# Kernel tuning notes

Hardware: AMD Instinct MI355X
Metric: run time of the kernel (lower is better)

Reference implementation:

```python
import jax, jax.numpy as jnp
import numpy as np

B = 8
INPUT_DIM = 6670   # upper-triangle of 116x116 FC matrix (AAL atlas)
N = 116
FD = 16
HEADS = (8, 4, 1)
DIMS = (128, 256, 512)
NC = 2
THR = 0.5
EPS = 1e-5


def _glorot(key, shape):
    s = (2.0 / (shape[0] + shape[-1])) ** 0.5
    return jax.random.normal(key, shape, dtype=jnp.float32) * s


def setup_inputs() -> dict:
    key = jax.random.key(0)
    ks = iter(jax.random.split(key, 64))
    inp = {}
    inp['x'] = jax.random.normal(next(ks), (B, INPUT_DIM), dtype=jnp.float32)
    # DynamicGraphBuilder params
    inp['W_gb'] = _glorot(next(ks), (INPUT_DIM, N * N))
    inp['b_gb'] = jnp.zeros((N * N,), jnp.float32)
    inp['fe_W1'] = _glorot(next(ks), (2, 8)); inp['fe_b1'] = jnp.zeros((8,), jnp.float32)
    inp['fe_W2'] = _glorot(next(ks), (8, FD)); inp['fe_b2'] = jnp.zeros((FD,), jnp.float32)
    inp['ln_g'] = jnp.ones((FD,), jnp.float32); inp['ln_b'] = jnp.zeros((FD,), jnp.float32)
    # GATv2 layers
    prev = FD
    for l, (d, h) in enumerate(zip(DIMS, HEADS)):
        inp['Wl%d' % l] = _glorot(next(ks), (prev, h * d))
        inp['bl%d' % l] = jnp.zeros((h * d,), jnp.float32)
        inp['Wr%d' % l] = _glorot(next(ks), (prev, h * d))
        inp['br%d' % l] = jnp.zeros((h * d,), jnp.float32)
        inp['att%d' % l] = _glorot(next(ks), (h, d))
        inp['bias%d' % l] = jnp.zeros((h * d,), jnp.float32)
        prev = h * d
    # classifier
    inp['Wc1'] = _glorot(next(ks), (prev, 256)); inp['bc1'] = jnp.zeros((256,), jnp.float32)
    inp['bn_g'] = jnp.ones((256,), jnp.float32); inp['bn_b'] = jnp.zeros((256,), jnp.float32)
    inp['Wc2'] = _glorot(next(ks), (256, NC)); inp['bc2'] = jnp.zeros((NC,), jnp.float32)
    return inp


def _gatv2(hx, mask_st, Wl, bl, Wr, br, att, bias, heads, out_dim, self_loops):
    # mask_st[b, src, tgt] True if edge src->tgt exists (PyG flow source_to_target)
    Bn, Nn, _ = hx.shape
    if self_loops:  # PyG remove_self_loops + add_self_loops => diag forced present
        mask_st = mask_st | jnp.eye(Nn, dtype=bool)
    xl = (hx @ Wl + bl).reshape(Bn, Nn, heads, out_dim)  # source transform
    xr = (hx @ Wr + br).reshape(Bn, Nn, heads, out_dim)  # target transform
    # pairwise: axis1 = target i, axis2 = source j  -> [B, i, j, h, o]
    z = jax.nn.leaky_relu(xr[:, :, None] + xl[:, None, :], 0.2)
    e = jnp.einsum('bijho,ho->bhij', z, att)  # [B, h, tgt, src]
    m = jnp.swapaxes(mask_st, 1, 2)[:, None]  # [B, 1, tgt, src]
    em = jnp.where(m, e, -1e30)
    emax = jnp.max(em, axis=-1, keepdims=True)
    p = jnp.exp(em - emax) * m  # zero for masked / empty rows
    alpha = p / jnp.maximum(p.sum(-1, keepdims=True), 1e-16)
    out = jnp.einsum('bhij,bjho->biho', alpha, xl).reshape(Bn, Nn, heads * out_dim)
    return out + bias


def _forward(x, W_gb, b_gb, fe_W1, fe_b1, fe_W2, fe_b2, ln_g, ln_b,
             Wl0, bl0, Wr0, br0, att0, bias0,
             Wl1, bl1, Wr1, br1, att1, bias1,
             Wl2, bl2, Wr2, br2, att2, bias2,
             Wc1, bc1, bn_g, bn_b, Wc2, bc2):
    Bn = x.shape[0]
    adj = jax.nn.sigmoid(x @ W_gb + b_gb).reshape(Bn, N, N)
    mask = adj > THR                      # edge (row -> col) exists
    adj_t = jnp.where(mask, adj, 0.0)     # thresholded adjacency
    mu = adj_t.mean(-1)                   # torch mean(dim=1) on [N,N]
    std = jnp.sqrt(jnp.sum((adj_t - mu[..., None]) ** 2, -1) / (N - 1))  # unbiased
    stats = jnp.stack([mu, std], -1)      # [B, N, 2]
    hfe = jax.nn.gelu(stats @ fe_W1 + fe_b1, approximate=False) @ fe_W2 + fe_b2
    lm = hfe.mean(-1, keepdims=True)
    lv = jnp.mean((hfe - lm) ** 2, -1, keepdims=True)
    h = (hfe - lm) / jnp.sqrt(lv + EPS) * ln_g + ln_b  # [B, N, FD]
    convs = [
        (Wl0, bl0, Wr0, br0, att0, bias0, HEADS[0], DIMS[0], False),
        (Wl1, bl1, Wr1, br1, att1, bias1, HEADS[1], DIMS[1], True),
        (Wl2, bl2, Wr2, br2, att2, bias2, HEADS[2], DIMS[2], True),
    ]
    for (Wl, bl, Wr, br, att, bias, hh, dd, sl) in convs:
        h = jax.nn.gelu(_gatv2(h, mask, Wl, bl, Wr, br, att, bias, hh, dd, sl), approximate=False)
    pooled = h.mean(1)                    # global_mean_pool per graph
    c = pooled @ Wc1 + bc1
    c = c / jnp.sqrt(1.0 + EPS) * bn_g + bn_b  # BatchNorm1d eval (running mean 0, var 1)
    c = jax.nn.gelu(c, approximate=False)
    return c @ Wc2 + bc2


def reference(x, W_gb, b_gb, fe_W1, fe_b1, fe_W2, fe_b2, ln_g, ln_b,
              Wl0, bl0, Wr0, br0, att0, bias0,
              Wl1, bl1, Wr1, br1, att1, bias1,
              Wl2, bl2, Wr2, br2, att2, bias2,
              Wc1, bc1, bn_g, bn_b, Wc2, bc2):
    return _forward(x, W_gb, b_gb, fe_W1, fe_b1, fe_W2, fe_b2, ln_g, ln_b,
                    Wl0, bl0, Wr0, br0, att0, bias0,
                    Wl1, bl1, Wr1, br1, att1, bias1,
                    Wl2, bl2, Wr2, br2, att2, bias2,
                    Wc1, bc1, bn_g, bn_b, Wc2, bc2)
```

## Files before the change

### kernel.cpp

```cpp
#include <hip/hip_runtime.h>
#include <math.h>


#define NB 8
#define NN 116
#define NN2 (NN*NN)
#define KIN 6670
#define FD 16
#define KCHUNK 64
#define KSTEP 105

__device__ __forceinline__ float gelu_f(float x) {
  return 0.5f * x * (1.0f + erff(x * 0.70710678118654752f));
}
__device__ __forceinline__ float lrelu(float x) {
  return fmaxf(x, 0.2f * x);
}

__global__ void k_transpose_x(const float* __restrict__ x, float* __restrict__ xT) {
  int idx = blockIdx.x * 256 + threadIdx.x;
  if (idx >= NB * KIN) return;
  int b = idx / KIN, k = idx % KIN;
  xT[k * NB + b] = x[idx];
}

__global__ __launch_bounds__(256) void k_gemm_big(
    const float* __restrict__ xT, const float* __restrict__ Wg,
    float* __restrict__ partial) {
  int c0 = (blockIdx.x * 256 + threadIdx.x) * 4;
  if (c0 >= NN2) return;
  int chunk = blockIdx.y;
  int k0 = chunk * KSTEP;
  int k1 = min(k0 + KSTEP, KIN);
  float acc[NB][4];
#pragma unroll
  for (int b = 0; b < NB; b++)
#pragma unroll
    for (int c = 0; c < 4; c++) acc[b][c] = 0.f;
#pragma unroll 4
  for (int k = k0; k < k1; ++k) {
    const float4 xa = *(const float4*)(xT + k * NB);
    const float4 xb = *(const float4*)(xT + k * NB + 4);
    float4 wv = *(const float4*)(Wg + (size_t)k * NN2 + c0);
    float w[4] = {wv.x, wv.y, wv.z, wv.w};
    float xs[NB] = {xa.x, xa.y, xa.z, xa.w, xb.x, xb.y, xb.z, xb.w};
#pragma unroll
    for (int b = 0; b < NB; b++)
#pragma unroll
      for (int c = 0; c < 4; c++)
        acc[b][c] = fmaf(xs[b], w[c], acc[b][c]);
  }
#pragma unroll
  for (int b = 0; b < NB; b++)
#pragma unroll
    for (int c = 0; c < 4; c++)
      partial[((size_t)chunk * NB + b) * NN2 + c0 + c] = acc[b][c];
}

__global__ void k_reduce_sigmoid(const float* __restrict__ partial,
                                 const float* __restrict__ bgb,
                                 float* __restrict__ adj) {
  int t = blockIdx.x * 256 + threadIdx.x;
  if (t >= NB * NN2) return;
  int b = t / NN2, rc = t % NN2;
  float s = bgb[rc];
#pragma unroll 8
  for (int ch = 0; ch < KCHUNK; ch++)
    s += partial[((size_t)ch * NB + b) * NN2 + rc];
  adj[t] = 1.0f / (1.0f + expf(-s));
}

__global__ void k_stats(const float* __restrict__ adj,
                        const float* __restrict__ feW1, const float* __restrict__ feb1,
                        const float* __restrict__ feW2, const float* __restrict__ feb2,
                        const float* __restrict__ lng, const float* __restrict__ lnb,
                        float* __restrict__ h0) {
  int b = blockIdx.x;
  int r = threadIdx.x;
  if (r >= NN) return;
  const float* row = adj + (size_t)(b * NN + r) * NN;
  float sum = 0.f;
  for (int c = 0; c < NN; c++) { float a = row[c]; sum += (a > 0.5f) ? a : 0.f; }
  float mu = sum / (float)NN;
  float ss = 0.f;
  for (int c = 0; c < NN; c++) {
    float a = row[c]; float m = (a > 0.5f) ? a : 0.f;
    float d = m - mu; ss += d * d;
  }
  float sd = sqrtf(ss / (float)(NN - 1));
  float hid[8];
#pragma unroll
  for (int a = 0; a < 8; a++) {
    float z = mu * feW1[a] + sd * feW1[8 + a] + feb1[a];
    hid[a] = gelu_f(z);
  }
  float hf[FD];
  float lm = 0.f;
#pragma unroll
  for (int o = 0; o < FD; o++) {
    float z = feb2[o];
#pragma unroll
    for (int a = 0; a < 8; a++) z += hid[a] * feW2[a * FD + o];
    hf[o] = z; lm += z;
  }
  lm /= (float)FD;
  float lv = 0.f;
#pragma unroll
  for (int o = 0; o < FD; o++) { float d = hf[o] - lm; lv += d * d; }
  lv /= (float)FD;
  float inv = 1.0f / sqrtf(lv + 1e-5f);
#pragma unroll
  for (int o = 0; o < FD; o++)
    h0[(size_t)(b * NN + r) * FD + o] = (hf[o] - lm) * inv * lng[o] + lnb[o];
}

#define GM 64
#define GN 64
#define GK 32
__global__ __launch_bounds__(256) void k_gemm_dual(
    const float* __restrict__ A,
    const float* __restrict__ W0, const float* __restrict__ b0,
    const float* __restrict__ W1, const float* __restrict__ b1,
    float* __restrict__ C0, float* __restrict__ C1,
    int M, int K, int N) {
  int nc = blockIdx.x * GN;
  const float* W    = (nc < N) ? W0 : W1;
  const float* bias = (nc < N) ? b0 : b1;
  float*       C    = (nc < N) ? C0 : C1;
  int n0 = (nc < N) ? nc : nc - N;
  int m0 = blockIdx.y * GM;

  __shared__ float a_s[GK][GM];
  __shared__ float b_s[GK][GN + 4];
  int t = threadIdx.x;
  int tx = t & 15, ty = t >> 4;
  float acc[4][4];
#pragma unroll
  for (int i = 0; i < 4; i++)
#pragma unroll
    for (int j = 0; j < 4; j++) acc[i][j] = 0.f;

  for (int kt = 0; kt < K; kt += GK) {
    {
      int m = t & 63, k8 = (t >> 6) * 8;
      int gm = m0 + m;
      float va[8];
      if (gm < M && (kt + k8 + 8) <= K) {
        float4 v0 = *(const float4*)(A + (size_t)gm * K + kt + k8);
        float4 v1 = *(const float4*)(A + (size_t)gm * K + kt + k8 + 4);
        va[0]=v0.x; va[1]=v0.y; va[2]=v0.z; va[3]=v0.w;
        va[4]=v1.x; va[5]=v1.y; va[6]=v1.z; va[7]=v1.w;
      } else {
#pragma unroll
        for (int e = 0; e < 8; e++) {
          int gk = kt + k8 + e;
          va[e] = (gm < M && gk < K) ? A[(size_t)gm * K + gk] : 0.f;
        }
      }
#pragma unroll
      for (int e = 0; e < 8; e++) a_s[k8 + e][m] = va[e];
    }
    {
      int k = t >> 3, n8 = (t & 7) * 8;
      int gk = kt + k;
      float4 w0 = make_float4(0.f,0.f,0.f,0.f), w1 = w0;
      if (gk < K) {
        const float* wp = W + (size_t)gk * N + n0 + n8;
        w0 = *(const float4*)(wp);
        w1 = *(const float4*)(wp + 4);
      }
      b_s[k][n8 + 0] = w0.x; b_s[k][n8 + 1] = w0.y;
      b_s[k][n8 + 2] = w0.z; b_s[k][n8 + 3] = w0.w;
      b_s[k][n8 + 4] = w1.x; b_s[k][n8 + 5] = w1.y;
      b_s[k][n8 + 6] = w1.z; b_s[k][n8 + 7] = w1.w;
    }
    __syncthreads();
#pragma unroll
    for (int kk = 0; kk < GK; kk++) {
      float4 av = *(const float4*)(&a_s[kk][ty << 2]);
      float4 bv = *(const float4*)(&b_s[kk][tx << 2]);
      float am[4] = {av.x, av.y, av.z, av.w};
      float bn_[4] = {bv.x, bv.y, bv.z, bv.w};
#pragma unroll
      for (int i = 0; i < 4; i++)
#pragma unroll
        for (int j = 0; j < 4; j++)
          acc[i][j] = fmaf(am[i], bn_[j], acc[i][j]);
    }
    __syncthreads();
  }
#pragma unroll
  for (int i = 0; i < 4; i++) {
    int m = m0 + (ty << 2) + i;
    if (m >= M) break;
#pragma unroll
    for (int j = 0; j < 4; j++) {
      int n = n0 + (tx << 2) + j;
      C[(size_t)m * N + n] = acc[i][j] + bias[n];
    }
  }
}

template<int HH_, int DD_>
__global__ __launch_bounds__(256) void k_attn_aggr(
    const float* __restrict__ xl, const float* __restrict__ xr,
    const float* __restrict__ adj, const float* __restrict__ att,
    const float* __restrict__ bias, float* __restrict__ hout, int selfloop) {
  constexpr int HD = HH_ * DD_;
  __shared__ float xr_lds[4][HD];
  __shared__ float att_lds[HD];
  __shared__ __align__(16) float e_lds[HH_][128][4];
  __shared__ float maskf[4][128];
  int i0 = blockIdx.x * 4, b = blockIdx.y;
  int t = threadIdx.x;

  for (int idx = t; idx < HD; idx += 256) {
    att_lds[idx] = att[idx];
#pragma unroll
    for (int ti = 0; ti < 4; ti++)
      xr_lds[ti][idx] = xr[(size_t)(b * NN + i0 + ti) * HD + idx];
  }
  if (t < 128) {
#pragma unroll
    for (int ti = 0; ti < 4; ti++) {
      int i = i0 + ti;
      bool mj = (t < NN) && ((adj[(size_t)(b * NN + t) * NN + i] > 0.5f) ||
                             (selfloop && (t == i)));
      maskf[ti][t] = mj ? 1.f : 0.f;
    }
  }
  __syncthreads();

  int half = t >> 7;
  int j = t & 127;
  bool valid = (j < NN);
  const float* xlj = xl + (size_t)(b * NN + (valid ? j : 0)) * HD;
  if constexpr (HH_ >= 2) {
    constexpr int HHH = HH_ / 2;
#pragma unroll
    for (int hh = 0; hh < HHH; hh++) {
      int h = half * HHH + hh;
      int base = h * DD_;
      float acc[4] = {0.f, 0.f, 0.f, 0.f};
      for (int o = 0; o < DD_; o += 4) {
        float4 v  = *(const float4*)(xlj + base + o);
        float4 af = *(const float4*)(att_lds + base + o);
#pragma unroll
        for (int ti = 0; ti < 4; ti++) {
          float4 r = *(const float4*)(&xr_lds[ti][base + o]);
          float a = acc[ti];
          a = fmaf(af.x, lrelu(r.x + v.x), a);
          a = fmaf(af.y, lrelu(r.y + v.y), a);
          a = fmaf(af.z, lrelu(r.z + v.z), a);
          a = fmaf(af.w, lrelu(r.w + v.w), a);
          acc[ti] = a;
        }
      }
      if (valid)
        *(float4*)(&e_lds[h][j][0]) = make_float4(acc[0], acc[1], acc[2], acc[3]);
    }
    __syncthreads();
  } else {
    constexpr int DH = DD_ / 2;
    int base = half * DH;
    float acc[4] = {0.f, 0.f, 0.f, 0.f};
    for (int o = 0; o < DH; o += 4) {
      float4 v  = *(const float4*)(xlj + base + o);
      float4 af = *(const float4*)(att_lds + base + o);
#pragma unroll
      for (int ti = 0; ti < 4; ti++) {
        float4 r = *(const float4*)(&xr_lds[ti][base + o]);
        float a = acc[ti];
        a = fmaf(af.x, lrelu(r.x + v.x), a);
        a = fmaf(af.y, lrelu(r.y + v.y), a);
        a = fmaf(af.z, lrelu(r.z + v.z), a);
        a = fmaf(af.w, lrelu(r.w + v.w), a);
        acc[ti] = a;
      }
    }
    if (half == 0 && valid)
      *(float4*)(&e_lds[0][j][0]) = make_float4(acc[0], acc[1], acc[2], acc[3]);
    __syncthreads();
    if (half == 1 && valid) {
      float4 p = *(const float4*)(&e_lds[0][j][0]);
      p.x += acc[0]; p.y += acc[1]; p.z += acc[2]; p.w += acc[3];
      *(float4*)(&e_lds[0][j][0]) = p;
    }
    __syncthreads();
  }

  {
    int w = t >> 6, lane = t & 63;
    for (int fh = w; fh < 4 * HH_; fh += 4) {
      int ti = fh / HH_, h = fh - ti * HH_;
      float mk0 = maskf[ti][lane], mk1 = maskf[ti][lane + 64];
      float e0 = e_lds[h][lane][ti], e1 = e_lds[h][lane + 64][ti];
      float v = fmaxf(mk0 != 0.f ? e0 : -3.0e38f,
                      mk1 != 0.f ? e1 : -3.0e38f);
#pragma unroll
      for (int o = 32; o; o >>= 1) v = fmaxf(v, __shfl_xor(v, o, 64));
      float p0 = (mk0 != 0.f) ? expf(e0 - v) : 0.f;
      float p1 = (mk1 != 0.f) ? expf(e1 - v) : 0.f;
      float s = p0 + p1;
#pragma unroll
      for (int o = 32; o; o >>= 1) s += __shfl_xor(s, o, 64);
      float inv = 1.0f / fmaxf(s, 1e-16f);
      e_lds[h][lane][ti]      = p0 * inv;
      e_lds[h][lane + 64][ti] = p1 * inv;
    }
  }
  __syncthreads();

  constexpr int CITER = HD / 256;
  const float* xb = xl + (size_t)b * NN * HD;
  float* hb = hout + (size_t)(b * NN + i0) * HD;
#pragma unroll
  for (int it = 0; it < CITER; it++) {
    int c = t + (it << 8);
    int h = c / DD_;
    const float* xp = xb + c;
    float a0 = 0.f, a1 = 0.f, a2 = 0.f, a3 = 0.f;
#pragma unroll 4
    for (int jj = 0; jj < NN; jj++) {
      float xv = xp[(size_t)jj * HD];
      float4 al = *(const float4*)(&e_lds[h][jj][0]);
      a0 = fmaf(al.x, xv, a0);
      a1 = fmaf(al.y, xv, a1);
      a2 = fmaf(al.z, xv, a2);
      a3 = fmaf(al.w, xv, a3);
    }
    float bv = bias[c];
    hb[c]          = gelu_f(a0 + bv);
    hb[HD + c]     = gelu_f(a1 + bv);
    hb[2 * HD + c] = gelu_f(a2 + bv);
    hb[3 * HD + c] = gelu_f(a3 + bv);
  }
}

__global__ __launch_bounds__(256) void k_classifier(
    const float* __restrict__ hfin,
    const float* __restrict__ Wc1, const float* __restrict__ bc1,
    const float* __restrict__ bng, const float* __restrict__ bnb,
    const float* __restrict__ Wc2, const float* __restrict__ bc2,
    float* __restrict__ out) {
  __shared__ float pooled[512];
  __shared__ float cls[256];
  int b = blockIdx.x;
  int t = threadIdx.x;
#pragma unroll
  for (int r = 0; r < 2; r++) {
    int c = t + (r << 8);
    float s = 0.f;
    for (int i = 0; i < NN; i++) s += hfin[(size_t)(b * NN + i) * 512 + c];
    pooled[c] = s / (float)NN;
  }
  __syncthreads();
  {
    int n = t;
    float acc = bc1[n];
    for (int k = 0; k < 512; k++)
      acc = fmaf(pooled[k], Wc1[k * 256 + n], acc);
    float c = acc * (1.0f / sqrtf(1.0f + 1e-5f)) * bng[n] + bnb[n];
    cls[n] = gelu_f(c);
  }
  __syncthreads();
  if (t < 128) {
    int jj = t >> 6, lane = t & 63;
    float s = 0.f;
#pragma unroll
    for (int w = 0; w < 4; w++) {
      int k = lane + (w << 6);
      s += cls[k] * Wc2[k * 2 + jj];
    }
#pragma unroll
    for (int o = 32; o; o >>= 1) s += __shfl_xor(s, o, 64);
    if (lane == 0) out[b * 2 + jj] = s + bc2[jj];
  }
}

extern "C" void kernel_launch(void* const* d_in, const int* in_sizes, int n_in,
                              void* d_out, int out_size, void* d_ws, size_t ws_size,
                              hipStream_t stream) {
  const float* x    = (const float*)d_in[0];
  const float* Wgb  = (const float*)d_in[1];
  const float* bgb  = (const float*)d_in[2];
  const float* feW1 = (const float*)d_in[3];
  const float* feb1 = (const float*)d_in[4];
  const float* feW2 = (const float*)d_in[5];
  const float* feb2 = (const float*)d_in[6];
  const float* lng  = (const float*)d_in[7];
  const float* lnb  = (const float*)d_in[8];
  const float* Wl[3]   = {(const float*)d_in[9],  (const float*)d_in[15], (const float*)d_in[21]};
  const float* bl[3]   = {(const float*)d_in[10], (const float*)d_in[16], (const float*)d_in[22]};
  const float* Wr[3]   = {(const float*)d_in[11], (const float*)d_in[17], (const float*)d_in[23]};
  const float* br[3]   = {(const float*)d_in[12], (const float*)d_in[18], (const float*)d_in[24]};
  const float* att[3]  = {(const float*)d_in[13], (const float*)d_in[19], (const float*)d_in[25]};
  const float* bias[3] = {(const float*)d_in[14], (const float*)d_in[20], (const float*)d_in[26]};
  const float* Wc1 = (const float*)d_in[27];
  const float* bc1 = (const float*)d_in[28];
  const float* bng = (const float*)d_in[29];
  const float* bnb = (const float*)d_in[30];
  const float* Wc2 = (const float*)d_in[31];
  const float* bc2 = (const float*)d_in[32];

  float* ws = (float*)d_ws;
  float* xT  = ws;
  float* adj = ws + 53376;
  float* scratch = ws + 161024;
  float* partial = scratch;
  float* hA      = scratch;
  float* hB      = hA + 950272;
  float* xlbuf   = hB + 950272;
  float* xrbuf   = xlbuf + 950272;

  k_transpose_x<<<dim3((NB * KIN + 255) / 256), 256, 0, stream>>>(x, xT);
  k_gemm_big<<<dim3(14, KCHUNK), 256, 0, stream>>>(xT, Wgb, partial);
  k_reduce_sigmoid<<<dim3((NB * NN2 + 255) / 256), 256, 0, stream>>>(partial, bgb, adj);
  k_stats<<<dim3(NB), 128, 0, stream>>>(adj, feW1, feb1, feW2, feb2, lng, lnb, hA);

  dim3 ab(NN / 4, NB);
  k_gemm_dual<<<dim3(2 * 1024 / GN, 15), 256, 0, stream>>>(
      hA, Wl[0], bl[0], Wr[0], br[0], xlbuf, xrbuf, 928, 16, 1024);
  k_attn_aggr<8, 128><<<ab, 256, 0, stream>>>(xlbuf, xrbuf, adj, att[0], bias[0], hB, 0);
  k_gemm_dual<<<dim3(2 * 1024 / GN, 15), 256, 0, stream>>>(
      hB, Wl[1], bl[1], Wr[1], br[1], xlbuf, xrbuf, 928, 1024, 1024);
  k_attn_aggr<4, 256><<<ab, 256, 0, stream>>>(xlbuf, xrbuf, adj, att[1], bias[1], hA, 1);
  k_gemm_dual<<<dim3(2 * 512 / GN, 15), 256, 0, stream>>>(
      hA, Wl[2], bl[2], Wr[2], br[2], xlbuf, xrbuf, 928, 1024, 512);
  k_attn_aggr<1, 512><<<ab, 256, 0, stream>>>(xlbuf, xrbuf, adj, att[2], bias[2], hB, 1);

  k_classifier<<<dim3(NB), 256, 0, stream>>>(hB, Wc1, bc1, bng, bnb, Wc2, bc2,
                                             (float*)d_out);
}
```

Before: 907.3 us.

## Drop x transpose, widen attention blocks to 512, template GEMM tile height

Removes the separate transpose kernel and has the big GEMM read x directly with scalar per-batch loads, with the k-loop unroll raised to 8. The dual projection GEMM is templated on tile height and uses a 128x64 tile with 8 rows per thread for the 1024x1024 layer. The attention kernels now launch 512 threads, spreading score computation, softmax and aggregation over more waves. This saves a launch and raises per-block parallelism, at the cost of uncoalesced x loads, more register pressure and fewer blocks for the middle GEMM.

```diff
diff --git a/kernel.cpp b/kernel.cpp
--- a/kernel.cpp
+++ b/kernel.cpp
@@ -17,15 +17,8 @@
   return fmaxf(x, 0.2f * x);
 }
 
-__global__ void k_transpose_x(const float* __restrict__ x, float* __restrict__ xT) {
-  int idx = blockIdx.x * 256 + threadIdx.x;
-  if (idx >= NB * KIN) return;
-  int b = idx / KIN, k = idx % KIN;
-  xT[k * NB + b] = x[idx];
-}
-
 __global__ __launch_bounds__(256) void k_gemm_big(
-    const float* __restrict__ xT, const float* __restrict__ Wg,
+    const float* __restrict__ x, const float* __restrict__ Wg,
     float* __restrict__ partial) {
   int c0 = (blockIdx.x * 256 + threadIdx.x) * 4;
   if (c0 >= NN2) return;
@@ -37,13 +30,13 @@
   for (int b = 0; b < NB; b++)
 #pragma unroll
     for (int c = 0; c < 4; c++) acc[b][c] = 0.f;
-#pragma unroll 4
+#pragma unroll 8
   for (int k = k0; k < k1; ++k) {
-    const float4 xa = *(const float4*)(xT + k * NB);
-    const float4 xb = *(const float4*)(xT + k * NB + 4);
     float4 wv = *(const float4*)(Wg + (size_t)k * NN2 + c0);
     float w[4] = {wv.x, wv.y, wv.z, wv.w};
-    float xs[NB] = {xa.x, xa.y, xa.z, xa.w, xb.x, xb.y, xb.z, xb.w};
+    float xs[NB];
+#pragma unroll
+    for (int b = 0; b < NB; b++) xs[b] = x[b * KIN + k];
 #pragma unroll
     for (int b = 0; b < NB; b++)
 #pragma unroll
@@ -114,9 +107,9 @@
     h0[(size_t)(b * NN + r) * FD + o] = (hf[o] - lm) * inv * lng[o] + lnb[o];
 }
 
-#define GM 64
 #define GN 64
 #define GK 32
+template<int GM_, int TM_>
 __global__ __launch_bounds__(256) void k_gemm_dual(
     const float* __restrict__ A,
     const float* __restrict__ W0, const float* __restrict__ b0,
@@ -128,37 +121,38 @@
   const float* bias = (nc < N) ? b0 : b1;
   float*       C    = (nc < N) ? C0 : C1;
   int n0 = (nc < N) ? nc : nc - N;
-  int m0 = blockIdx.y * GM;
-
-  __shared__ float a_s[GK][GM];
+  int m0 = blockIdx.y * GM_;
+
+  __shared__ float a_s[GK][GM_];
   __shared__ float b_s[GK][GN + 4];
   int t = threadIdx.x;
   int tx = t & 15, ty = t >> 4;
-  float acc[4][4];
-#pragma unroll
-  for (int i = 0; i < 4; i++)
+  float acc[TM_][4];
+#pragma unroll
+  for (int i = 0; i < TM_; i++)
 #pragma unroll
     for (int j = 0; j < 4; j++) acc[i][j] = 0.f;
+
+  constexpr int EPT = GM_ * GK / 256;
 
   for (int kt = 0; kt < K; kt += GK) {
     {
-      int m = t & 63, k8 = (t >> 6) * 8;
+      int m = t & (GM_ - 1), kq = (t / GM_) * EPT;
       int gm = m0 + m;
-      float va[8];
-      if (gm < M && (kt + k8 + 8) <= K) {
-        float4 v0 = *(const float4*)(A + (size_t)gm * K + kt + k8);
-        float4 v1 = *(const float4*)(A + (size_t)gm * K + kt + k8 + 4);
-        va[0]=v0.x; va[1]=v0.y; va[2]=v0.z; va[3]=v0.w;
-        va[4]=v1.x; va[5]=v1.y; va[6]=v1.z; va[7]=v1.w;
+      if (gm < M && (kt + kq + EPT) <= K) {
+#pragma unroll
+        for (int e = 0; e < EPT; e += 4) {
+          float4 v = *(const float4*)(A + (size_t)gm * K + kt + kq + e);
+          a_s[kq + e + 0][m] = v.x; a_s[kq + e + 1][m] = v.y;
+          a_s[kq + e + 2][m] = v.z; a_s[kq + e + 3][m] = v.w;
+        }
       } else {
 #pragma unroll
-        for (int e = 0; e < 8; e++) {
-          int gk = kt + k8 + e;
-          va[e] = (gm < M && gk < K) ? A[(size_t)gm * K + gk] : 0.f;
+        for (int e = 0; e < EPT; e++) {
+          int gk = kt + kq + e;
+          a_s[kq + e][m] = (gm < M && gk < K) ? A[(size_t)gm * K + gk] : 0.f;
         }
       }
-#pragma unroll
-      for (int e = 0; e < 8; e++) a_s[k8 + e][m] = va[e];
     }
     {
       int k = t >> 3, n8 = (t & 7) * 8;
@@ -177,21 +171,24 @@
     __syncthreads();
 #pragma unroll
     for (int kk = 0; kk < GK; kk++) {
-      float4 av = *(const float4*)(&a_s[kk][ty << 2]);
       float4 bv = *(const float4*)(&b_s[kk][tx << 2]);
-      float am[4] = {av.x, av.y, av.z, av.w};
       float bn_[4] = {bv.x, bv.y, bv.z, bv.w};
 #pragma unroll
-      for (int i = 0; i < 4; i++)
-#pragma unroll
-        for (int j = 0; j < 4; j++)
-          acc[i][j] = fmaf(am[i], bn_[j], acc[i][j]);
+      for (int r = 0; r < TM_ / 4; r++) {
+        float4 av = *(const float4*)(&a_s[kk][ty * TM_ + r * 4]);
+        float am[4] = {av.x, av.y, av.z, av.w};
+#pragma unroll
+        for (int i = 0; i < 4; i++)
+#pragma unroll
+          for (int j = 0; j < 4; j++)
+            acc[r * 4 + i][j] = fmaf(am[i], bn_[j], acc[r * 4 + i][j]);
+      }
     }
     __syncthreads();
   }
 #pragma unroll
-  for (int i = 0; i < 4; i++) {
-    int m = m0 + (ty << 2) + i;
+  for (int i = 0; i < TM_; i++) {
+    int m = m0 + ty * TM_ + i;
     if (m >= M) break;
 #pragma unroll
     for (int j = 0; j < 4; j++) {
@@ -202,7 +199,7 @@
 }
 
 template<int HH_, int DD_>
-__global__ __launch_bounds__(256) void k_attn_aggr(
+__global__ __launch_bounds__(512) void k_attn_aggr(
     const float* __restrict__ xl, const float* __restrict__ xr,
     const float* __restrict__ adj, const float* __restrict__ att,
     const float* __restrict__ bias, float* __restrict__ hout, int selfloop) {
@@ -214,7 +211,7 @@
   int i0 = blockIdx.x * 4, b = blockIdx.y;
   int t = threadIdx.x;
 
-  for (int idx = t; idx < HD; idx += 256) {
+  for (int idx = t; idx < HD; idx += 512) {
     att_lds[idx] = att[idx];
 #pragma unroll
     for (int ti = 0; ti < 4; ti++)
@@ -231,15 +228,15 @@
   }
   __syncthreads();
 
-  int half = t >> 7;
+  int slice = t >> 7;
   int j = t & 127;
   bool valid = (j < NN);
   const float* xlj = xl + (size_t)(b * NN + (valid ? j : 0)) * HD;
-  if constexpr (HH_ >= 2) {
-    constexpr int HHH = HH_ / 2;
-#pragma unroll
-    for (int hh = 0; hh < HHH; hh++) {
-      int h = half * HHH + hh;
+  if constexpr (HH_ >= 4) {
+    constexpr int HQ = HH_ / 4;
+#pragma unroll
+    for (int hh = 0; hh < HQ; hh++) {
+      int h = slice * HQ + hh;
       int base = h * DD_;
       float acc[4] = {0.f, 0.f, 0.f, 0.f};
       for (int o = 0; o < DD_; o += 4) {
@@ -262,26 +259,28 @@
     __syncthreads();
   } else {
     constexpr int DH = DD_ / 2;
-    int base = half * DH;
     float acc[4] = {0.f, 0.f, 0.f, 0.f};
-    for (int o = 0; o < DH; o += 4) {
-      float4 v  = *(const float4*)(xlj + base + o);
-      float4 af = *(const float4*)(att_lds + base + o);
-#pragma unroll
-      for (int ti = 0; ti < 4; ti++) {
-        float4 r = *(const float4*)(&xr_lds[ti][base + o]);
-        float a = acc[ti];
-        a = fmaf(af.x, lrelu(r.x + v.x), a);
-        a = fmaf(af.y, lrelu(r.y + v.y), a);
-        a = fmaf(af.z, lrelu(r.z + v.z), a);
-        a = fmaf(af.w, lrelu(r.w + v.w), a);
-        acc[ti] = a;
+    if (slice < 2) {
+      int base = slice * DH;
+      for (int o = 0; o < DH; o += 4) {
+        float4 v  = *(const float4*)(xlj + base + o);
+        float4 af = *(const float4*)(att_lds + base + o);
+#pragma unroll
+        for (int ti = 0; ti < 4; ti++) {
+          float4 r = *(const float4*)(&xr_lds[ti][base + o]);
+          float a = acc[ti];
+          a = fmaf(af.x, lrelu(r.x + v.x), a);
+          a = fmaf(af.y, lrelu(r.y + v.y), a);
+          a = fmaf(af.z, lrelu(r.z + v.z), a);
+          a = fmaf(af.w, lrelu(r.w + v.w), a);
+          acc[ti] = a;
+        }
       }
     }
-    if (half == 0 && valid)
+    if (slice == 0 && valid)
       *(float4*)(&e_lds[0][j][0]) = make_float4(acc[0], acc[1], acc[2], acc[3]);
     __syncthreads();
-    if (half == 1 && valid) {
+    if (slice == 1 && valid) {
       float4 p = *(const float4*)(&e_lds[0][j][0]);
       p.x += acc[0]; p.y += acc[1]; p.z += acc[2]; p.w += acc[3];
       *(float4*)(&e_lds[0][j][0]) = p;
@@ -291,7 +290,7 @@
 
   {
     int w = t >> 6, lane = t & 63;
-    for (int fh = w; fh < 4 * HH_; fh += 4) {
+    for (int fh = w; fh < 4 * HH_; fh += 8) {
       int ti = fh / HH_, h = fh - ti * HH_;
       float mk0 = maskf[ti][lane], mk1 = maskf[ti][lane + 64];
       float e0 = e_lds[h][lane][ti], e1 = e_lds[h][lane + 64][ti];
@@ -311,12 +310,12 @@
   }
   __syncthreads();
 
-  constexpr int CITER = HD / 256;
+  constexpr int CITER = HD / 512;
   const float* xb = xl + (size_t)b * NN * HD;
   float* hb = hout + (size_t)(b * NN + i0) * HD;
 #pragma unroll
   for (int it = 0; it < CITER; it++) {
-    int c = t + (it << 8);
+    int c = t + (it << 9);
     int h = c / DD_;
     const float* xp = xb + c;
     float a0 = 0.f, a1 = 0.f, a2 = 0.f, a3 = 0.f;
@@ -404,7 +403,6 @@
   const float* bc2 = (const float*)d_in[32];
 
   float* ws = (float*)d_ws;
-  float* xT  = ws;
   float* adj = ws + 53376;
   float* scratch = ws + 161024;
   float* partial = scratch;
@@ -413,21 +411,20 @@
   float* xlbuf   = hB + 950272;
   float* xrbuf   = xlbuf + 950272;
 
-  k_transpose_x<<<dim3((NB * KIN + 255) / 256), 256, 0, stream>>>(x, xT);
-  k_gemm_big<<<dim3(14, KCHUNK), 256, 0, stream>>>(xT, Wgb, partial);
+  k_gemm_big<<<dim3(14, KCHUNK), 256, 0, stream>>>(x, Wgb, partial);
   k_reduce_sigmoid<<<dim3((NB * NN2 + 255) / 256), 256, 0, stream>>>(partial, bgb, adj);
   k_stats<<<dim3(NB), 128, 0, stream>>>(adj, feW1, feb1, feW2, feb2, lng, lnb, hA);
 
   dim3 ab(NN / 4, NB);
-  k_gemm_dual<<<dim3(2 * 1024 / GN, 15), 256, 0, stream>>>(
+  k_gemm_dual<64, 4><<<dim3(2 * 1024 / GN, 15), 256, 0, stream>>>(
       hA, Wl[0], bl[0], Wr[0], br[0], xlbuf, xrbuf, 928, 16, 1024);
-  k_attn_aggr<8, 128><<<ab, 256, 0, stream>>>(xlbuf, xrbuf, adj, att[0], bias[0], hB, 0);
-  k_gemm_dual<<<dim3(2 * 1024 / GN, 15), 256, 0, stream>>>(
+  k_attn_aggr<8, 128><<<ab, 512, 0, stream>>>(xlbuf, xrbuf, adj, att[0], bias[0], hB, 0);
+  k_gemm_dual<128, 8><<<dim3(2 * 1024 / GN, 8), 256, 0, stream>>>(
       hB, Wl[1], bl[1], Wr[1], br[1], xlbuf, xrbuf, 928, 1024, 1024);
-  k_attn_aggr<4, 256><<<ab, 256, 0, stream>>>(xlbuf, xrbuf, adj, att[1], bias[1], hA, 1);
-  k_gemm_dual<<<dim3(2 * 512 / GN, 15), 256, 0, stream>>>(
+  k_attn_aggr<4, 256><<<ab, 512, 0, stream>>>(xlbuf, xrbuf, adj, att[1], bias[1], hA, 1);
+  k_gemm_dual<64, 4><<<dim3(2 * 512 / GN, 15), 256, 0, stream>>>(
       hA, Wl[2], bl[2], Wr[2], br[2], xlbuf, xrbuf, 928, 1024, 512);
-  k_attn_aggr<1, 512><<<ab, 256, 0, stream>>>(xlbuf, xrbuf, adj, att[2], bias[2], hB, 1);
+  k_attn_aggr<1, 512><<<ab, 512, 0, stream>>>(xlbuf, xrbuf, adj, att[2], bias[2], hB, 1);
 
   k_classifier<<<dim3(NB), 256, 0, stream>>>(hB, Wc1, bc1, bng, bnb, Wc2, bc2,
                                              (float*)d_out);
```

Result: no change. 895.4 us (-1.3%).
